# Performance work log

Hardware: AMD Instinct MI355X
Metric: run time of the kernel (lower is better)

The kernel has to match this reference:

```python
import jax, jax.numpy as jnp
import numpy as np

N, C, D, H, O = 8192, 100, 128, 128, 64


def setup_inputs() -> dict:
    key = jax.random.key(0)
    k1, k2, k3, k4 = jax.random.split(key, 4)
    x = jax.random.normal(k1, (N, D), dtype=jnp.float32)
    cat_ids = jax.random.randint(k2, (N,), 0, C)
    W1 = 0.02 * jax.random.normal(k3, (C, D, H), dtype=jnp.float32)
    b1 = jnp.zeros((C, H), dtype=jnp.float32)
    W2 = 0.02 * jax.random.normal(k4, (C, H, O), dtype=jnp.float32)
    b2 = jnp.zeros((C, O), dtype=jnp.float32)
    return {"x": x, "cat_ids": cat_ids, "W1": W1, "b1": b1, "W2": W2, "b2": b2}


def reference(x, cat_ids, W1, b1, W2, b2):
    # Layer 1: per-token category-weight gather + matmul + bias, then ReLU.
    # selected_W1: [N, D, H] (the large gathered intermediate, as in the torch code)
    h = jax.nn.relu(jnp.einsum('nd,ndh->nh', x, W1[cat_ids]) + b1[cat_ids])
    # Layer 2: [N, H] x [N, H, O] -> [N, O]
    out = jnp.einsum('nh,nho->no', h, W2[cat_ids]) + b2[cat_ids]
    return out
```

## Files before the change

kernel.cpp:

```cpp
#include <hip/hip_runtime.h>


#define N_TOK 8192
#define C_CAT 100
#define D_IN  128
#define H_MID 128
#define O_OUT 64
#define TPB   64
#define MAX_ITEMS (C_CAT + N_TOK / TPB)


typedef __attribute__((ext_vector_type(8))) short short8;
typedef __attribute__((ext_vector_type(4))) float floatx4;

__global__ __launch_bounds__(256) void zero_kernel(int* __restrict__ ws) {
  ws[threadIdx.x] = 0;
}

__global__ __launch_bounds__(256) void hist_kernel(
    const int* __restrict__ cat_ids, int* __restrict__ ws) {
  __shared__ int h[C_CAT];
  int t = threadIdx.x;
  if (t < C_CAT) h[t] = 0;
  __syncthreads();
  int g = blockIdx.x * 256 + t;
  atomicAdd(&h[cat_ids[g]], 1);
  __syncthreads();
  if (t < C_CAT && h[t] > 0) atomicAdd(&ws[t], h[t]);
}

__global__ __launch_bounds__(128) void scan_kernel(int* __restrict__ ws) {
  __shared__ int sc[128], sk[128];
  int t = threadIdx.x;
  int v  = (t < C_CAT) ? ws[t] : 0;
  int ck = (v + TPB - 1) / TPB;
  sc[t] = v; sk[t] = ck;
  __syncthreads();
  for (int off = 1; off < 128; off <<= 1) {
    int a = 0, b = 0;
    if (t >= off) { a = sc[t - off]; b = sk[t - off]; }
    __syncthreads();
    sc[t] += a; sk[t] += b;
    __syncthreads();
  }
  if (t < C_CAT) {
    int start = sc[t] - v;
    int ibase = sk[t] - ck;
    ws[128 + t] = start;
    int* items = ws + 272;
    for (int k = 0; k < ck; ++k) {
      items[3 * (ibase + k) + 0] = t;
      items[3 * (ibase + k) + 1] = start + k * TPB;
      items[3 * (ibase + k) + 2] = min(TPB, v - k * TPB);
    }
  }
  if (t == 127) ws[256] = sk[127];
}

__global__ __launch_bounds__(256) void scatter_kernel(
    const int* __restrict__ cat_ids, int* __restrict__ ws) {
  __shared__ int lcnt[C_CAT];
  __shared__ int gbase[C_CAT];
  int t = threadIdx.x;
  if (t < C_CAT) lcnt[t] = 0;
  __syncthreads();
  int g = blockIdx.x * 256 + t;
  int c = cat_ids[g];
  int r = atomicAdd(&lcnt[c], 1);
  __syncthreads();
  if (t < C_CAT && lcnt[t] > 0) gbase[t] = atomicAdd(&ws[128 + t], lcnt[t]);
  __syncthreads();
  ws[2048 + gbase[c] + r] = g;
}

__device__ __forceinline__ void bf16_split(float f, short& hi, short& lo) {
  unsigned b  = __builtin_bit_cast(unsigned, f);
  unsigned hb = b & 0xFFFF0000u;
  hi = (short)(hb >> 16);
  float r = f - __builtin_bit_cast(float, hb);
  unsigned rb = __builtin_bit_cast(unsigned, r);
  lo = (short)((rb + 0x7FFFu + ((rb >> 16) & 1u)) >> 16);
}

__device__ __forceinline__ void split8(const float* v, short8& h8, short8& l8) {
  #pragma unroll
  for (int j = 0; j < 8; ++j) { short hh, ll; bf16_split(v[j], hh, ll); h8[j] = hh; l8[j] = ll; }
}

__global__ __launch_bounds__(256, 1) void mlp_kernel(
    const float* __restrict__ x,  const float* __restrict__ W1,
    const float* __restrict__ b1, const float* __restrict__ W2,
    const float* __restrict__ b2, float* __restrict__ out,
    const int* __restrict__ ws) {
  int bid = blockIdx.x;
  if (bid >= ws[256]) return;
  const int* item = ws + 272 + 3 * bid;
  int cat = item[0], start = item[1], cnt = item[2];
  const int* sorted = ws + 2048;

  __shared__ __align__(16) short XF[2][8192];
  __shared__ int toks[TPB];

  int tid  = threadIdx.x;
  int lane = tid & 63;
  int wv   = tid >> 6;

  if (tid < TPB) toks[tid] = sorted[start + min(tid, cnt - 1)];

  int mrow = (wv << 4) + (lane & 15);
  int tok  = sorted[start + (mrow < cnt ? mrow : 0)];
  const float* xr = x + (size_t)tok * D_IN + ((lane >> 4) << 3);
  float xq[4][8];
  #pragma unroll
  for (int p = 0; p < 4; ++p) {
    *(float4*)&xq[p][0] = *(const float4*)(xr + (p << 5));
    *(float4*)&xq[p][4] = *(const float4*)(xr + (p << 5) + 4);
  }

  const float* W1c = W1 + (size_t)cat * (D_IN * H_MID);
  float w1a[4][8], w1b[4][8];
  #pragma unroll
  for (int p = 0; p < 4; ++p) {
    int f   = (p << 2) + wv;
    int nt  = f & 7;
    int ksl = f >> 3;
    int n   = (nt << 4) + (lane & 15);
    int kb  = (ksl << 5) + ((lane >> 4) << 3);
    #pragma unroll
    for (int j = 0; j < 8; ++j) {
      w1a[p][j] = W1c[(size_t)(kb + j) * H_MID + n];
      w1b[p][j] = W1c[(size_t)(64 + kb + j) * H_MID + n];
    }
  }

  const float* W2c = W2 + (size_t)cat * (H_MID * O_OUT);
  float w2r[4][8];
  {
    int n = (wv << 4) + (lane & 15);
    #pragma unroll
    for (int p = 0; p < 4; ++p) {
      int kb = (p << 5) + ((lane >> 4) << 3);
      #pragma unroll
      for (int j = 0; j < 8; ++j)
        w2r[p][j] = W2c[(size_t)(kb + j) * O_OUT + n];
    }
  }

  float b1v[2];
  #pragma unroll
  for (int ntl = 0; ntl < 2; ++ntl) {
    int ntile = wv + (ntl << 2);
    b1v[ntl] = b1[(size_t)cat * H_MID + (ntile << 4) + (lane & 15)];
  }
  float b2v = b2[(size_t)cat * O_OUT + (wv << 4) + (lane & 15)];

  #pragma unroll
  for (int p = 0; p < 4; ++p) {
    short8 h8, l8;
    split8(xq[p], h8, l8);
    int f = (p << 2) + wv;
    ((short8*)XF[0])[(f << 6) + lane] = h8;
    ((short8*)XF[1])[(f << 6) + lane] = l8;
  }
  __syncthreads();

  floatx4 acc[4][2];
  #pragma unroll
  for (int mt = 0; mt < 4; ++mt)
    #pragma unroll
    for (int ntl = 0; ntl < 2; ++ntl) acc[mt][ntl] = 0.f;

  #pragma unroll
  for (int ksg = 0; ksg < 4; ++ksg) {
    short8 ah[4], al[4];
    #pragma unroll
    for (int mt = 0; mt < 4; ++mt) {
      ah[mt] = ((short8*)XF[0])[(((ksg << 2) + mt) << 6) + lane];
      al[mt] = ((short8*)XF[1])[(((ksg << 2) + mt) << 6) + lane];
    }
    short8 bh[2], bl[2];
    #pragma unroll
    for (int ntl = 0; ntl < 2; ++ntl) {
      const float* wreg = (ksg < 2) ? w1a[((ksg & 1) << 1) + ntl]
                                    : w1b[((ksg & 1) << 1) + ntl];
      split8(wreg, bh[ntl], bl[ntl]);
    }
    #pragma unroll
    for (int mt = 0; mt < 4; ++mt)
      #pragma unroll
      for (int ntl = 0; ntl < 2; ++ntl) {
        acc[mt][ntl] = __builtin_amdgcn_mfma_f32_16x16x32_bf16(ah[mt], bh[ntl], acc[mt][ntl], 0, 0, 0);
        acc[mt][ntl] = __builtin_amdgcn_mfma_f32_16x16x32_bf16(ah[mt], bl[ntl], acc[mt][ntl], 0, 0, 0);
        acc[mt][ntl] = __builtin_amdgcn_mfma_f32_16x16x32_bf16(al[mt], bh[ntl], acc[mt][ntl], 0, 0, 0);
      }
  }
  __syncthreads();

  #pragma unroll
  for (int ntl = 0; ntl < 2; ++ntl) {
    int ntile = wv + (ntl << 2);
    int n = (ntile << 4) + (lane & 15);
    #pragma unroll
    for (int mt = 0; mt < 4; ++mt) {
      #pragma unroll
      for (int r = 0; r < 4; ++r) {
        float hfull = fmaxf(acc[mt][ntl][r] + b1v[ntl], 0.f);
        short hh, hl; bf16_split(hfull, hh, hl);
        int m  = (mt << 4) + ((lane >> 4) << 2) + r;
        int f2 = ((n >> 5) << 2) + mt;
        int L2 = (((n >> 3) & 3) << 4) + (m & 15);
        int sa = (f2 << 9) + (L2 << 3) + (n & 7);
        XF[0][sa] = hh; XF[1][sa] = hl;
      }
    }
  }
  __syncthreads();

  floatx4 acc2[4];
  #pragma unroll
  for (int mt = 0; mt < 4; ++mt) acc2[mt] = 0.f;

  #pragma unroll
  for (int ks = 0; ks < 4; ++ks) {
    short8 bh, bl;
    split8(w2r[ks], bh, bl);
    #pragma unroll
    for (int mt = 0; mt < 4; ++mt) {
      short8 ah = ((short8*)XF[0])[(((ks << 2) + mt) << 6) + lane];
      short8 al = ((short8*)XF[1])[(((ks << 2) + mt) << 6) + lane];
      acc2[mt] = __builtin_amdgcn_mfma_f32_16x16x32_bf16(ah, bh, acc2[mt], 0, 0, 0);
      acc2[mt] = __builtin_amdgcn_mfma_f32_16x16x32_bf16(ah, bl, acc2[mt], 0, 0, 0);
      acc2[mt] = __builtin_amdgcn_mfma_f32_16x16x32_bf16(al, bh, acc2[mt], 0, 0, 0);
    }
  }

  {
    int n2 = (wv << 4) + (lane & 15);
    #pragma unroll
    for (int mt = 0; mt < 4; ++mt) {
      #pragma unroll
      for (int r = 0; r < 4; ++r) {
        int m = (mt << 4) + ((lane >> 4) << 2) + r;
        if (m < cnt)
          out[(size_t)toks[m] * O_OUT + n2] = acc2[mt][r] + b2v;
      }
    }
  }
}

extern "C" void kernel_launch(void* const* d_in, const int* in_sizes, int n_in,
                              void* d_out, int out_size, void* d_ws, size_t ws_size,
                              hipStream_t stream) {
  const float* x       = (const float*)d_in[0];
  const int*   cat_ids = (const int*)  d_in[1];
  const float* W1      = (const float*)d_in[2];
  const float* b1      = (const float*)d_in[3];
  const float* W2      = (const float*)d_in[4];
  const float* b2      = (const float*)d_in[5];
  float* out = (float*)d_out;
  int*   ws  = (int*)d_ws;

  zero_kernel   <<<1,            256, 0, stream>>>(ws);
  hist_kernel   <<<N_TOK / 256,  256, 0, stream>>>(cat_ids, ws);
  scan_kernel   <<<1,            128, 0, stream>>>(ws);
  scatter_kernel<<<N_TOK / 256,  256, 0, stream>>>(cat_ids, ws);
  mlp_kernel    <<<MAX_ITEMS,    256, 0, stream>>>(x, W1, b1, W2, b2, out, ws);
}
```

Before: 89.44 us.

## Fuse token bucketing into MLP kernel, each block scanning cat_ids for its category

Removes the zero/histogram/scan/scatter kernels and the workspace. Each of 200 blocks (two per category) scans all cat_ids to count and locate its category's tokens, then loops over 64-token chunks with the category weights held in registers. This eliminates four extra kernel launches and the global atomics, at the cost of every block redundantly reading the full 32KB id array and running a shared-memory prefix scan. Weights are now loaded once per block rather than once per chunk.

```diff
diff --git a/kernel.cpp b/kernel.cpp
--- a/kernel.cpp
+++ b/kernel.cpp
@@ -6,72 +6,11 @@
 #define D_IN  128
 #define H_MID 128
 #define O_OUT 64
-#define TPB   64
-#define MAX_ITEMS (C_CAT + N_TOK / TPB)
-
+#define NCHUNK 2
+#define GRID (C_CAT * NCHUNK)
 
 typedef __attribute__((ext_vector_type(8))) short short8;
 typedef __attribute__((ext_vector_type(4))) float floatx4;
-
-__global__ __launch_bounds__(256) void zero_kernel(int* __restrict__ ws) {
-  ws[threadIdx.x] = 0;
-}
-
-__global__ __launch_bounds__(256) void hist_kernel(
-    const int* __restrict__ cat_ids, int* __restrict__ ws) {
-  __shared__ int h[C_CAT];
-  int t = threadIdx.x;
-  if (t < C_CAT) h[t] = 0;
-  __syncthreads();
-  int g = blockIdx.x * 256 + t;
-  atomicAdd(&h[cat_ids[g]], 1);
-  __syncthreads();
-  if (t < C_CAT && h[t] > 0) atomicAdd(&ws[t], h[t]);
-}
-
-__global__ __launch_bounds__(128) void scan_kernel(int* __restrict__ ws) {
-  __shared__ int sc[128], sk[128];
-  int t = threadIdx.x;
-  int v  = (t < C_CAT) ? ws[t] : 0;
-  int ck = (v + TPB - 1) / TPB;
-  sc[t] = v; sk[t] = ck;
-  __syncthreads();
-  for (int off = 1; off < 128; off <<= 1) {
-    int a = 0, b = 0;
-    if (t >= off) { a = sc[t - off]; b = sk[t - off]; }
-    __syncthreads();
-    sc[t] += a; sk[t] += b;
-    __syncthreads();
-  }
-  if (t < C_CAT) {
-    int start = sc[t] - v;
-    int ibase = sk[t] - ck;
-    ws[128 + t] = start;
-    int* items = ws + 272;
-    for (int k = 0; k < ck; ++k) {
-      items[3 * (ibase + k) + 0] = t;
-      items[3 * (ibase + k) + 1] = start + k * TPB;
-      items[3 * (ibase + k) + 2] = min(TPB, v - k * TPB);
-    }
-  }
-  if (t == 127) ws[256] = sk[127];
-}
-
-__global__ __launch_bounds__(256) void scatter_kernel(
-    const int* __restrict__ cat_ids, int* __restrict__ ws) {
-  __shared__ int lcnt[C_CAT];
-  __shared__ int gbase[C_CAT];
-  int t = threadIdx.x;
-  if (t < C_CAT) lcnt[t] = 0;
-  __syncthreads();
-  int g = blockIdx.x * 256 + t;
-  int c = cat_ids[g];
-  int r = atomicAdd(&lcnt[c], 1);
-  __syncthreads();
-  if (t < C_CAT && lcnt[t] > 0) gbase[t] = atomicAdd(&ws[128 + t], lcnt[t]);
-  __syncthreads();
-  ws[2048 + gbase[c] + r] = g;
-}
 
 __device__ __forceinline__ void bf16_split(float f, short& hi, short& lo) {
   unsigned b  = __builtin_bit_cast(unsigned, f);
@@ -88,34 +27,20 @@
 }
 
 __global__ __launch_bounds__(256, 1) void mlp_kernel(
-    const float* __restrict__ x,  const float* __restrict__ W1,
-    const float* __restrict__ b1, const float* __restrict__ W2,
-    const float* __restrict__ b2, float* __restrict__ out,
-    const int* __restrict__ ws) {
-  int bid = blockIdx.x;
-  if (bid >= ws[256]) return;
-  const int* item = ws + 272 + 3 * bid;
-  int cat = item[0], start = item[1], cnt = item[2];
-  const int* sorted = ws + 2048;
-
-  __shared__ __align__(16) short XF[2][8192];
-  __shared__ int toks[TPB];
-
+    const float* __restrict__ x,  const int* __restrict__ cat_ids,
+    const float* __restrict__ W1, const float* __restrict__ b1,
+    const float* __restrict__ W2, const float* __restrict__ b2,
+    float* __restrict__ out) {
+  int bid  = blockIdx.x;
+  int cat  = bid >> 1;
+  int j0   = bid & 1;
   int tid  = threadIdx.x;
   int lane = tid & 63;
   int wv   = tid >> 6;
 
-  if (tid < TPB) toks[tid] = sorted[start + min(tid, cnt - 1)];
-
-  int mrow = (wv << 4) + (lane & 15);
-  int tok  = sorted[start + (mrow < cnt ? mrow : 0)];
-  const float* xr = x + (size_t)tok * D_IN + ((lane >> 4) << 3);
-  float xq[4][8];
-  #pragma unroll
-  for (int p = 0; p < 4; ++p) {
-    *(float4*)&xq[p][0] = *(const float4*)(xr + (p << 5));
-    *(float4*)&xq[p][4] = *(const float4*)(xr + (p << 5) + 4);
-  }
+  __shared__ __align__(16) short XF[2][8192];
+  __shared__ int toks[64];
+  __shared__ int sc[256];
 
   const float* W1c = W1 + (size_t)cat * (D_IN * H_MID);
   float w1a[4][8], w1b[4][8];
@@ -132,7 +57,6 @@
       w1b[p][j] = W1c[(size_t)(64 + kb + j) * H_MID + n];
     }
   }
-
   const float* W2c = W2 + (size_t)cat * (H_MID * O_OUT);
   float w2r[4][8];
   {
@@ -145,104 +69,148 @@
         w2r[p][j] = W2c[(size_t)(kb + j) * O_OUT + n];
     }
   }
-
   float b1v[2];
   #pragma unroll
-  for (int ntl = 0; ntl < 2; ++ntl) {
-    int ntile = wv + (ntl << 2);
-    b1v[ntl] = b1[(size_t)cat * H_MID + (ntile << 4) + (lane & 15)];
-  }
+  for (int ntl = 0; ntl < 2; ++ntl)
+    b1v[ntl] = b1[(size_t)cat * H_MID + ((wv + (ntl << 2)) << 4) + (lane & 15)];
   float b2v = b2[(size_t)cat * O_OUT + (wv << 4) + (lane & 15)];
 
-  #pragma unroll
-  for (int p = 0; p < 4; ++p) {
-    short8 h8, l8;
-    split8(xq[p], h8, l8);
-    int f = (p << 2) + wv;
-    ((short8*)XF[0])[(f << 6) + lane] = h8;
-    ((short8*)XF[1])[(f << 6) + lane] = l8;
-  }
+  const int4* cid4 = (const int4*)cat_ids;
+  int mycnt = 0;
+  #pragma unroll
+  for (int k = 0; k < 8; ++k) {
+    int4 v = cid4[tid + (k << 8)];
+    mycnt += (v.x == cat) + (v.y == cat) + (v.z == cat) + (v.w == cat);
+  }
+  sc[tid] = mycnt;
   __syncthreads();
-
-  floatx4 acc[4][2];
-  #pragma unroll
-  for (int mt = 0; mt < 4; ++mt)
-    #pragma unroll
-    for (int ntl = 0; ntl < 2; ++ntl) acc[mt][ntl] = 0.f;
-
-  #pragma unroll
-  for (int ksg = 0; ksg < 4; ++ksg) {
-    short8 ah[4], al[4];
-    #pragma unroll
-    for (int mt = 0; mt < 4; ++mt) {
-      ah[mt] = ((short8*)XF[0])[(((ksg << 2) + mt) << 6) + lane];
-      al[mt] = ((short8*)XF[1])[(((ksg << 2) + mt) << 6) + lane];
-    }
-    short8 bh[2], bl[2];
+  for (int off = 1; off < 256; off <<= 1) {
+    int a = (tid >= off) ? sc[tid - off] : 0;
+    __syncthreads();
+    sc[tid] += a;
+    __syncthreads();
+  }
+  int TOT   = sc[255];
+  int ebase = sc[tid] - mycnt;
+
+  for (int chunk = j0; (chunk << 6) < TOT; chunk += NCHUNK) {
+    int ccnt = min(64, TOT - (chunk << 6));
+    __syncthreads();
+    if (tid < 64) toks[tid] = 0;
+    __syncthreads();
+    {
+      int r = ebase, lo = chunk << 6;
+      #pragma unroll
+      for (int k = 0; k < 8; ++k) {
+        int4 v = cid4[tid + (k << 8)];
+        int p = (tid + (k << 8)) << 2;
+        if (v.x == cat) { int rel = r - lo; if ((unsigned)rel < 64u) toks[rel] = p;     ++r; }
+        if (v.y == cat) { int rel = r - lo; if ((unsigned)rel < 64u) toks[rel] = p + 1; ++r; }
+        if (v.z == cat) { int rel = r - lo; if ((unsigned)rel < 64u) toks[rel] = p + 2; ++r; }
+        if (v.w == cat) { int rel = r - lo; if ((unsigned)rel < 64u) toks[rel] = p + 3; ++r; }
+      }
+    }
+    __syncthreads();
+
+    int mrow = (wv << 4) + (lane & 15);
+    int tok  = toks[mrow];
+    const float* xr = x + (size_t)tok * D_IN + ((lane >> 4) << 3);
+    float xq[4][8];
+    #pragma unroll
+    for (int p = 0; p < 4; ++p) {
+      *(float4*)&xq[p][0] = *(const float4*)(xr + (p << 5));
+      *(float4*)&xq[p][4] = *(const float4*)(xr + (p << 5) + 4);
+    }
+    #pragma unroll
+    for (int p = 0; p < 4; ++p) {
+      short8 h8, l8;
+      split8(xq[p], h8, l8);
+      int f = (p << 2) + wv;
+      ((short8*)XF[0])[(f << 6) + lane] = h8;
+      ((short8*)XF[1])[(f << 6) + lane] = l8;
+    }
+    __syncthreads();
+
+    floatx4 acc[4][2];
+    #pragma unroll
+    for (int mt = 0; mt < 4; ++mt)
+      #pragma unroll
+      for (int ntl = 0; ntl < 2; ++ntl) acc[mt][ntl] = 0.f;
+
+    #pragma unroll
+    for (int ksg = 0; ksg < 4; ++ksg) {
+      short8 ah[4], al[4];
+      #pragma unroll
+      for (int mt = 0; mt < 4; ++mt) {
+        ah[mt] = ((short8*)XF[0])[(((ksg << 2) + mt) << 6) + lane];
+        al[mt] = ((short8*)XF[1])[(((ksg << 2) + mt) << 6) + lane];
+      }
+      short8 bh[2], bl[2];
+      #pragma unroll
+      for (int ntl = 0; ntl < 2; ++ntl) {
+        const float* wreg = (ksg < 2) ? w1a[((ksg & 1) << 1) + ntl]
+                                      : w1b[((ksg & 1) << 1) + ntl];
+        split8(wreg, bh[ntl], bl[ntl]);
+      }
+      #pragma unroll
+      for (int mt = 0; mt < 4; ++mt)
+        #pragma unroll
+        for (int ntl = 0; ntl < 2; ++ntl) {
+          acc[mt][ntl] = __builtin_amdgcn_mfma_f32_16x16x32_bf16(ah[mt], bh[ntl], acc[mt][ntl], 0, 0, 0);
+          acc[mt][ntl] = __builtin_amdgcn_mfma_f32_16x16x32_bf16(ah[mt], bl[ntl], acc[mt][ntl], 0, 0, 0);
+          acc[mt][ntl] = __builtin_amdgcn_mfma_f32_16x16x32_bf16(al[mt], bh[ntl], acc[mt][ntl], 0, 0, 0);
+        }
+    }
+    __syncthreads();
+
     #pragma unroll
     for (int ntl = 0; ntl < 2; ++ntl) {
-      const float* wreg = (ksg < 2) ? w1a[((ksg & 1) << 1) + ntl]
-                                    : w1b[((ksg & 1) << 1) + ntl];
-      split8(wreg, bh[ntl], bl[ntl]);
-    }
-    #pragma unroll
-    for (int mt = 0; mt < 4; ++mt)
-      #pragma unroll
-      for (int ntl = 0; ntl < 2; ++ntl) {
-        acc[mt][ntl] = __builtin_amdgcn_mfma_f32_16x16x32_bf16(ah[mt], bh[ntl], acc[mt][ntl], 0, 0, 0);
-        acc[mt][ntl] = __builtin_amdgcn_mfma_f32_16x16x32_bf16(ah[mt], bl[ntl], acc[mt][ntl], 0, 0, 0);
-        acc[mt][ntl] = __builtin_amdgcn_mfma_f32_16x16x32_bf16(al[mt], bh[ntl], acc[mt][ntl], 0, 0, 0);
-      }
-  }
-  __syncthreads();
-
-  #pragma unroll
-  for (int ntl = 0; ntl < 2; ++ntl) {
-    int ntile = wv + (ntl << 2);
-    int n = (ntile << 4) + (lane & 15);
-    #pragma unroll
-    for (int mt = 0; mt < 4; ++mt) {
-      #pragma unroll
-      for (int r = 0; r < 4; ++r) {
-        float hfull = fmaxf(acc[mt][ntl][r] + b1v[ntl], 0.f);
-        short hh, hl; bf16_split(hfull, hh, hl);
-        int m  = (mt << 4) + ((lane >> 4) << 2) + r;
-        int f2 = ((n >> 5) << 2) + mt;
-        int L2 = (((n >> 3) & 3) << 4) + (m & 15);
-        int sa = (f2 << 9) + (L2 << 3) + (n & 7);
-        XF[0][sa] = hh; XF[1][sa] = hl;
-      }
-    }
-  }
-  __syncthreads();
-
-  floatx4 acc2[4];
-  #pragma unroll
-  for (int mt = 0; mt < 4; ++mt) acc2[mt] = 0.f;
-
-  #pragma unroll
-  for (int ks = 0; ks < 4; ++ks) {
-    short8 bh, bl;
-    split8(w2r[ks], bh, bl);
-    #pragma unroll
-    for (int mt = 0; mt < 4; ++mt) {
-      short8 ah = ((short8*)XF[0])[(((ks << 2) + mt) << 6) + lane];
-      short8 al = ((short8*)XF[1])[(((ks << 2) + mt) << 6) + lane];
-      acc2[mt] = __builtin_amdgcn_mfma_f32_16x16x32_bf16(ah, bh, acc2[mt], 0, 0, 0);
-      acc2[mt] = __builtin_amdgcn_mfma_f32_16x16x32_bf16(ah, bl, acc2[mt], 0, 0, 0);
-      acc2[mt] = __builtin_amdgcn_mfma_f32_16x16x32_bf16(al, bh, acc2[mt], 0, 0, 0);
-    }
-  }
-
-  {
-    int n2 = (wv << 4) + (lane & 15);
-    #pragma unroll
-    for (int mt = 0; mt < 4; ++mt) {
-      #pragma unroll
-      for (int r = 0; r < 4; ++r) {
-        int m = (mt << 4) + ((lane >> 4) << 2) + r;
-        if (m < cnt)
-          out[(size_t)toks[m] * O_OUT + n2] = acc2[mt][r] + b2v;
+      int ntile = wv + (ntl << 2);
+      int n = (ntile << 4) + (lane & 15);
+      #pragma unroll
+      for (int mt = 0; mt < 4; ++mt) {
+        #pragma unroll
+        for (int r = 0; r < 4; ++r) {
+          float hfull = fmaxf(acc[mt][ntl][r] + b1v[ntl], 0.f);
+          short hh, hl; bf16_split(hfull, hh, hl);
+          int m  = (mt << 4) + ((lane >> 4) << 2) + r;
+          int f2 = ((n >> 5) << 2) + mt;
+          int L2 = (((n >> 3) & 3) << 4) + (m & 15);
+          int sa = (f2 << 9) + (L2 << 3) + (n & 7);
+          XF[0][sa] = hh; XF[1][sa] = hl;
+        }
+      }
+    }
+    __syncthreads();
+
+    floatx4 acc2[4];
+    #pragma unroll
+    for (int mt = 0; mt < 4; ++mt) acc2[mt] = 0.f;
+
+    #pragma unroll
+    for (int ks = 0; ks < 4; ++ks) {
+      short8 bh, bl;
+      split8(w2r[ks], bh, bl);
+      #pragma unroll
+      for (int mt = 0; mt < 4; ++mt) {
+        short8 ah = ((short8*)XF[0])[(((ks << 2) + mt) << 6) + lane];
+        short8 al = ((short8*)XF[1])[(((ks << 2) + mt) << 6) + lane];
+        acc2[mt] = __builtin_amdgcn_mfma_f32_16x16x32_bf16(ah, bh, acc2[mt], 0, 0, 0);
+        acc2[mt] = __builtin_amdgcn_mfma_f32_16x16x32_bf16(ah, bl, acc2[mt], 0, 0, 0);
+        acc2[mt] = __builtin_amdgcn_mfma_f32_16x16x32_bf16(al, bh, acc2[mt], 0, 0, 0);
+      }
+    }
+
+    {
+      int n2 = (wv << 4) + (lane & 15);
+      #pragma unroll
+      for (int mt = 0; mt < 4; ++mt) {
+        #pragma unroll
+        for (int r = 0; r < 4; ++r) {
+          int m = (mt << 4) + ((lane >> 4) << 2) + r;
+          if (m < ccnt)
+            out[(size_t)toks[m] * O_OUT + n2] = acc2[mt][r] + b2v;
+        }
       }
     }
   }
@@ -258,11 +226,6 @@
   const float* W2      = (const float*)d_in[4];
   const float* b2      = (const float*)d_in[5];
   float* out = (float*)d_out;
-  int*   ws  = (int*)d_ws;
-
-  zero_kernel   <<<1,            256, 0, stream>>>(ws);
-  hist_kernel   <<<N_TOK / 256,  256, 0, stream>>>(cat_ids, ws);
-  scan_kernel   <<<1,            128, 0, stream>>>(ws);
-  scatter_kernel<<<N_TOK / 256,  256, 0, stream>>>(cat_ids, ws);
-  mlp_kernel    <<<MAX_ITEMS,    256, 0, stream>>>(x, W1, b1, W2, b2, out, ws);
-}
+
+  mlp_kernel<<<GRID, 256, 0, stream>>>(x, cat_ids, W1, b1, W2, b2, out);
+}
```

After: 81.80 us. 1.09x faster.
